# Kernel optimization log

Measured on AMD Instinct MI355X. Metric: run time of the kernel, lower is better.

The kernel has to match this reference:

```python
import jax, jax.numpy as jnp
import numpy as np

D_MODEL = 1024
N_HEAD = 16
HEAD_DIM = D_MODEL // N_HEAD
D_FF = int(D_MODEL * 4.0)
B, T = 2, 2048


def rms_norm(x, eps=1e-6):
    return x * jax.lax.rsqrt(jnp.mean(jnp.square(x), axis=-1, keepdims=True) + eps)


def rope_tables(T, head_dim):
    # half-truncated RoPE: first quarter of dims get real freqs, next quarter zeros
    angular_freq = (1.0 / 1024.0) ** jnp.linspace(0.0, 1.0, head_dim // 4, dtype=jnp.float32)
    angular_freq = jnp.concatenate([angular_freq, jnp.zeros(head_dim // 4, jnp.float32)])
    theta = jnp.arange(T, dtype=jnp.float32)[:, None] * angular_freq[None, :]  # [T, head_dim//2]
    return jnp.cos(theta), jnp.sin(theta)


def apply_rope(x, cos, sin):
    # x: [B, H, T, D]; cos/sin: [T, D//2]
    x1, x2 = jnp.split(x.astype(jnp.float32), 2, axis=-1)
    c = cos[None, None]
    s = sin[None, None]
    y1 = x1 * c + x2 * s
    y2 = -x1 * s + x2 * c
    return jnp.concatenate([y1, y2], axis=-1).astype(x.dtype)


def setup_inputs() -> dict:
    key = jax.random.key(0)
    ks = jax.random.split(key, 10)
    x = jax.random.normal(ks[0], (B, T, D_MODEL), jnp.float32)
    block_mask = jnp.tril(jnp.ones((T, T), jnp.bool_))  # causal
    sc = 1.0 / np.sqrt(D_MODEL)
    Wqkv = jax.random.normal(ks[1], (D_MODEL, 3 * D_MODEL), jnp.float32) * sc
    bqkv = jnp.zeros((3 * D_MODEL,), jnp.float32)
    Wo = jax.random.normal(ks[2], (D_MODEL, D_MODEL), jnp.float32) * sc
    bo = jnp.zeros((D_MODEL,), jnp.float32)
    W1 = jax.random.normal(ks[3], (D_MODEL, D_FF), jnp.float32) * sc
    b1 = jnp.zeros((D_FF,), jnp.float32)
    W2 = jax.random.normal(ks[4], (D_FF, D_MODEL), jnp.float32) * (1.0 / np.sqrt(D_FF))
    b2 = jnp.zeros((D_MODEL,), jnp.float32)
    return {"x": x, "block_mask": block_mask, "Wqkv": Wqkv, "bqkv": bqkv,
            "Wo": Wo, "bo": bo, "W1": W1, "b1": b1, "W2": W2, "b2": b2}


def reference(x, block_mask, Wqkv, bqkv, Wo, bo, W1, b1, W2, b2):
    Bq, Tq, D = x.shape
    cos, sin = rope_tables(Tq, HEAD_DIM)

    def attn(h):
        qkv = h @ Wqkv + bqkv  # [B, T, 3D]
        qkv = qkv.reshape(Bq, Tq, 3, N_HEAD, HEAD_DIM)
        qkv = jnp.transpose(qkv, (2, 0, 3, 1, 4))  # [3, B, H, T, d]
        q, k, v = qkv[0], qkv[1], qkv[2]
        q, k = rms_norm(q), rms_norm(k)
        q, k = apply_rope(q, cos, sin), apply_rope(k, cos, sin)
        scores = jnp.einsum('bhtd,bhsd->bhts', q, k) / np.sqrt(HEAD_DIM)
        scores = jnp.where(block_mask[None, None], scores, jnp.float32(-1e30))
        p = jax.nn.softmax(scores, axis=-1)
        o = jnp.einsum('bhts,bhsd->bhtd', p, v)
        o = jnp.transpose(o, (0, 2, 1, 3)).reshape(Bq, Tq, D)
        return o @ Wo + bo

    def mlp(h):
        return jax.nn.gelu(h @ W1 + b1) @ W2 + b2

    x = x + attn(rms_norm(x))
    x = x + mlp(rms_norm(x))
    return x
```

## Files before the change

### kernel.cpp

```cpp
#include <hip/hip_runtime.h>
#include <hip/hip_bf16.h>


typedef __attribute__((ext_vector_type(8))) short short8;
typedef __attribute__((ext_vector_type(4))) float f32x4;
typedef __attribute__((ext_vector_type(8))) unsigned short u16x8;

#define MROWS 4096
#define DMODEL 1024
#define DFF 4096
#define NH 16
#define HD 64
#define SEQ 2048

static __device__ __forceinline__ unsigned short f2bf(float f) {
    union { __hip_bfloat16 b; unsigned short u; } cv;
    cv.b = __float2bfloat16(f);
    return cv.u;
}

static __device__ __forceinline__ void gload_lds16(const void* g, void* l) {
    __builtin_amdgcn_global_load_lds(
        (const __attribute__((address_space(1))) unsigned int*)g,
        (__attribute__((address_space(3))) unsigned int*)l, 16, 0, 0);
}

__global__ void cast_transpose(const float* __restrict__ W,
                               unsigned short* __restrict__ Wt, int K, int N) {
    __shared__ float tile[32][33];
    const int tx = threadIdx.x & 31;
    const int ty = threadIdx.x >> 5;
    const int n0 = blockIdx.x * 32, k0 = blockIdx.y * 32;
#pragma unroll
    for (int i = 0; i < 4; ++i) {
        int kk = ty + i * 8;
        tile[kk][tx] = W[(long)(k0 + kk) * N + n0 + tx];
    }
    __syncthreads();
#pragma unroll
    for (int i = 0; i < 4; ++i) {
        int nn = ty + i * 8;
        Wt[(long)(n0 + nn) * K + k0 + tx] = f2bf(tile[tx][nn]);
    }
}

__global__ void rope_table(float* __restrict__ cosT, float* __restrict__ sinT) {
    const int t = blockIdx.x, j = threadIdx.x;
    float th = (j < 16) ? (float)t * exp2f(-(10.0f / 15.0f) * (float)j) : 0.0f;
    cosT[t * 32 + j] = cosf(th);
    sinT[t * 32 + j] = sinf(th);
}

__global__ void rmsnorm_cast(const float* __restrict__ xin,
                             unsigned short* __restrict__ hout) {
    const int row = blockIdx.x;
    const float4 v = ((const float4*)(xin + (long)row * DMODEL))[threadIdx.x];
    float ss = v.x * v.x + v.y * v.y + v.z * v.z + v.w * v.w;
#pragma unroll
    for (int m = 32; m >= 1; m >>= 1) ss += __shfl_xor(ss, m);
    __shared__ float part[4];
    if ((threadIdx.x & 63) == 0) part[threadIdx.x >> 6] = ss;
    __syncthreads();
    const float tot = part[0] + part[1] + part[2] + part[3];
    const float sc = rsqrtf(tot * (1.0f / (float)DMODEL) + 1e-6f);
    ushort4 o;
    o.x = f2bf(v.x * sc); o.y = f2bf(v.y * sc);
    o.z = f2bf(v.z * sc); o.w = f2bf(v.w * sc);
    ((ushort4*)hout)[(long)row * (DMODEL / 4) + threadIdx.x] = o;
}

template <int EPI>
__launch_bounds__(256)
__global__ void gemm_bt(const short* __restrict__ A, const short* __restrict__ Bt,
                        const float* __restrict__ bias, const float* __restrict__ res,
                        float* __restrict__ outF, unsigned short* __restrict__ outB,
                        int N, int K) {
    __shared__ short As[128 * 32];
    __shared__ short Bs[128 * 32];
    const int tid = threadIdx.x;
    const int lane = tid & 63, w = tid >> 6;
    const int wr = w >> 1, wc = w & 1;
    const int l16 = lane & 15, lhi = lane >> 4;
    const long rowA0 = (long)blockIdx.y * 128;
    const long rowB0 = (long)blockIdx.x * 128;

    const f32x4 fz = {0.f, 0.f, 0.f, 0.f};
    f32x4 acc[4][4];
#pragma unroll
    for (int m = 0; m < 4; ++m)
#pragma unroll
        for (int n = 0; n < 4; ++n) acc[m][n] = fz;

    const int ktiles = K >> 5;
    for (int kt = 0; kt < ktiles; ++kt) {
        const int k0 = kt << 5;
#pragma unroll
        for (int it = 0; it < 2; ++it) {
            const int cbase = it * 256 + w * 64;
            const int c = cbase + lane;
            const int r = c >> 2, col = (c & 3) << 3;
            gload_lds16(A + (rowA0 + r) * K + k0 + col,
                        (char*)As + cbase * 16 + lane * 16);
            gload_lds16(Bt + (rowB0 + r) * K + k0 + col,
                        (char*)Bs + cbase * 16 + lane * 16);
        }
        __syncthreads();
        short8 af[4], bf[4];
#pragma unroll
        for (int m = 0; m < 4; ++m)
            af[m] = *(const short8*)(As + (wr * 64 + m * 16 + l16) * 32 + lhi * 8);
#pragma unroll
        for (int n = 0; n < 4; ++n)
            bf[n] = *(const short8*)(Bs + (wc * 64 + n * 16 + l16) * 32 + lhi * 8);
#pragma unroll
        for (int m = 0; m < 4; ++m)
#pragma unroll
            for (int n = 0; n < 4; ++n)
                acc[m][n] = __builtin_amdgcn_mfma_f32_16x16x32_bf16(
                    af[m], bf[n], acc[m][n], 0, 0, 0);
        __syncthreads();
    }

#pragma unroll
    for (int m = 0; m < 4; ++m) {
        const long r0 = rowA0 + wr * 64 + m * 16 + lhi * 4;
#pragma unroll
        for (int n = 0; n < 4; ++n) {
            const long cc = rowB0 + wc * 64 + n * 16 + l16;
            const float bv = bias[cc];
#pragma unroll
            for (int j = 0; j < 4; ++j) {
                const long idx = (r0 + j) * N + cc;
                float v = acc[m][n][j] + bv;
                if (EPI == 1) v += res[idx];
                if (EPI == 2) {
                    float g = 0.5f * v *
                        (1.0f + tanhf(0.7978845608028654f * (v + 0.044715f * v * v * v)));
                    outB[idx] = f2bf(g);
                } else {
                    outF[idx] = v;
                }
            }
        }
    }
}

__global__ void qkv_post(const float* __restrict__ qkv, const float* __restrict__ cosT,
                         const float* __restrict__ sinT, unsigned short* __restrict__ Qo,
                         unsigned short* __restrict__ Ko) {
    const int lane = threadIdx.x & 63;
    const int g = blockIdx.x * 4 + (threadIdx.x >> 6);
    const int row = g >> 4, h = g & 15;
    const int b = row >> 11, t = row & 2047;
    const float* base = qkv + (long)row * 3072 + h * 64;
    float q = base[lane];
    float k = base[1024 + lane];
    float sq = q * q, sk = k * k;
#pragma unroll
    for (int m = 32; m >= 1; m >>= 1) {
        sq += __shfl_xor(sq, m);
        sk += __shfl_xor(sk, m);
    }
    q *= rsqrtf(sq * (1.0f / 64.0f) + 1e-6f);
    k *= rsqrtf(sk * (1.0f / 64.0f) + 1e-6f);
    const int j = lane & 31;
    const float c = cosT[t * 32 + j], s = sinT[t * 32 + j];
    const float q2 = __shfl_xor(q, 32), k2 = __shfl_xor(k, 32);
    const float sgn = (lane < 32) ? 1.0f : -1.0f;
    const float qr = q * c + sgn * q2 * s;
    const float kr = k * c + sgn * k2 * s;
    const long o = ((long)(b * 16 + h) * SEQ + t) * 64 + lane;
    Qo[o] = f2bf(qr * 0.125f);
    Ko[o] = f2bf(kr);
}

__global__ void transpose_v(const float* __restrict__ qkv,
                            unsigned short* __restrict__ Vt) {
    __shared__ float tile[64][65];
    const int tid = threadIdx.x;
    const int bh = blockIdx.x, tt = blockIdx.y;
    const int b = bh >> 4, h = bh & 15;
    const int tr = tid >> 2, c0 = (tid & 3) * 16;
    const float* src = qkv + ((long)(b * SEQ + tt * 64 + tr)) * 3072 + 2048 + h * 64 + c0;
#pragma unroll
    for (int i = 0; i < 4; ++i) {
        float4 v = ((const float4*)src)[i];
        tile[tr][c0 + i * 4 + 0] = v.x;
        tile[tr][c0 + i * 4 + 1] = v.y;
        tile[tr][c0 + i * 4 + 2] = v.z;
        tile[tr][c0 + i * 4 + 3] = v.w;
    }
    __syncthreads();
    const int d = tid >> 2, t0 = (tid & 3) * 16;
    unsigned short* dst = Vt + ((long)bh * 64 + d) * SEQ + tt * 64 + t0;
#pragma unroll
    for (int half = 0; half < 2; ++half) {
        u16x8 o;
#pragma unroll
        for (int e = 0; e < 8; ++e) o[e] = f2bf(tile[t0 + half * 8 + e][d]);
        *(u16x8*)(dst + half * 8) = o;
    }
}

__launch_bounds__(256)
__global__ void attn_fwd(const short* __restrict__ Qg, const short* __restrict__ Kg,
                         const short* __restrict__ Vtg, unsigned short* __restrict__ Og) {
    __shared__ short Ks[64 * 64];
    __shared__ short Vs[64 * 64];
    __shared__ char Ps[4][16 * 128];
    const int tid = threadIdx.x, lane = tid & 63, w = tid >> 6;
    const int l16 = lane & 15, lhi = lane >> 4;
    const int bh = blockIdx.x;
    const int qt = 31 - blockIdx.y;
    const int bb = bh >> 4, hh = bh & 15;
    const long base_q = (long)bh * (SEQ * 64);

    short8 aq0, aq1;
    {
        const short* Qp = Qg + base_q + (long)(qt * 64 + w * 16) * 64;
        aq0 = *(const short8*)(Qp + l16 * 64 + lhi * 8);
        aq1 = *(const short8*)(Qp + l16 * 64 + 32 + lhi * 8);
    }
    float mrow[4] = {-1e30f, -1e30f, -1e30f, -1e30f};
    float lrow[4] = {0.f, 0.f, 0.f, 0.f};
    const f32x4 fz = {0.f, 0.f, 0.f, 0.f};
    f32x4 oacc[4];
#pragma unroll
    for (int n = 0; n < 4; ++n) oacc[n] = fz;

    char* Pw = &Ps[w][0];

    for (int kt = 0; kt <= qt; ++kt) {
        const short* Kp = Kg + base_q + (long)kt * 64 * 64;
        const short* Vp = Vtg + base_q + (long)kt * 64;
#pragma unroll
        for (int it = 0; it < 2; ++it) {
            const int cbase = it * 256 + w * 64;
            const int c = cbase + lane;
            const int r = c >> 3;
            const int col = ((c & 7) ^ (r & 7)) << 3;
            gload_lds16(Kp + r * 64 + col, (char*)Ks + c * 16);
            gload_lds16(Vp + (long)r * SEQ + col, (char*)Vs + c * 16);
        }
        __syncthreads();

        f32x4 s[4];
        __builtin_amdgcn_s_setprio(1);
#pragma unroll
        for (int n = 0; n < 4; ++n) {
            const int kr = n * 16 + l16;
            short8 bk0 = *(const short8*)(Ks + kr * 64 + ((lhi ^ (kr & 7)) << 3));
            short8 bk1 = *(const short8*)(Ks + kr * 64 + (((lhi + 4) ^ (kr & 7)) << 3));
            f32x4 z = fz;
            z = __builtin_amdgcn_mfma_f32_16x16x32_bf16(aq0, bk0, z, 0, 0, 0);
            s[n] = __builtin_amdgcn_mfma_f32_16x16x32_bf16(aq1, bk1, z, 0, 0, 0);
        }
        __builtin_amdgcn_s_setprio(0);
        if (kt == qt) {
#pragma unroll
            for (int n = 0; n < 4; ++n)
#pragma unroll
                for (int j = 0; j < 4; ++j)
                    if (n * 16 + l16 > w * 16 + lhi * 4 + j) s[n][j] = -1e30f;
        }

#pragma unroll
        for (int j = 0; j < 4; ++j) {
            float pm = fmaxf(fmaxf(s[0][j], s[1][j]), fmaxf(s[2][j], s[3][j]));
            pm = fmaxf(pm, __shfl_xor(pm, 1));
            pm = fmaxf(pm, __shfl_xor(pm, 2));
            pm = fmaxf(pm, __shfl_xor(pm, 4));
            pm = fmaxf(pm, __shfl_xor(pm, 8));
            const float newm = fmaxf(mrow[j], pm);
            const float sc = __expf(mrow[j] - newm);
            float ps = 0.f;
#pragma unroll
            for (int n = 0; n < 4; ++n) {
                float p = __expf(s[n][j] - newm);
                s[n][j] = p;
                ps += p;
            }
            ps += __shfl_xor(ps, 1);
            ps += __shfl_xor(ps, 2);
            ps += __shfl_xor(ps, 4);
            ps += __shfl_xor(ps, 8);
            lrow[j] = lrow[j] * sc + ps;
            mrow[j] = newm;
#pragma unroll
            for (int n = 0; n < 4; ++n) oacc[n][j] *= sc;
        }

#pragma unroll
        for (int n = 0; n < 4; ++n)
#pragma unroll
            for (int j = 0; j < 4; ++j) {
                const int q = lhi * 4 + j, colp = n * 16 + l16;
                *(short*)(Pw + ((q * 128 + colp * 2) ^ ((q & 7) << 4))) =
                    (short)f2bf(s[n][j]);
            }
        __builtin_amdgcn_s_setprio(1);
#pragma unroll
        for (int ks = 0; ks < 2; ++ks) {
            short8 pa = *(const short8*)(Pw + ((l16 * 128 + ks * 64 + lhi * 16) ^ ((l16 & 7) << 4)));
#pragma unroll
            for (int n = 0; n < 4; ++n) {
                const int dr = n * 16 + l16;
                short8 vb = *(const short8*)(Vs + dr * 64 + ((((ks << 2) + lhi) ^ (dr & 7)) << 3));
                oacc[n] = __builtin_amdgcn_mfma_f32_16x16x32_bf16(pa, vb, oacc[n], 0, 0, 0);
            }
        }
        __builtin_amdgcn_s_setprio(0);
        __syncthreads();
    }

#pragma unroll
    for (int n = 0; n < 4; ++n)
#pragma unroll
        for (int j = 0; j < 4; ++j) {
            const int qrow = qt * 64 + w * 16 + lhi * 4 + j;
            const long orow = (long)bb * SEQ + qrow;
            const int col = hh * 64 + n * 16 + l16;
            Og[orow * DMODEL + col] = f2bf(oacc[n][j] / lrow[j]);
        }
}

extern "C" void kernel_launch(void* const* d_in, const int* in_sizes, int n_in,
                              void* d_out, int out_size, void* d_ws, size_t ws_size,
                              hipStream_t stream) {
    const float* x    = (const float*)d_in[0];
    const float* Wqkv = (const float*)d_in[2];
    const float* bqkv = (const float*)d_in[3];
    const float* Wo   = (const float*)d_in[4];
    const float* bo   = (const float*)d_in[5];
    const float* W1   = (const float*)d_in[6];
    const float* b1   = (const float*)d_in[7];
    const float* W2   = (const float*)d_in[8];
    const float* b2   = (const float*)d_in[9];
    float* out = (float*)d_out;

    char* ws = (char*)d_ws;
    auto alloc = [&](size_t b) {
        char* p = ws;
        ws += (b + 255) & ~(size_t)255;
        return p;
    };
    short* WqkvT = (short*)alloc(3072ull * 1024 * 2);
    short* WoT   = (short*)alloc(1024ull * 1024 * 2);
    short* W1T   = (short*)alloc(4096ull * 1024 * 2);
    short* W2T   = (short*)alloc(1024ull * 4096 * 2);
    float* cosT  = (float*)alloc(2048ull * 32 * 4);
    float* sinT  = (float*)alloc(2048ull * 32 * 4);
    short* hbuf  = (short*)alloc((size_t)MROWS * DMODEL * 2);
    short* Qb    = (short*)alloc(32ull * SEQ * 64 * 2);
    short* Kb    = (short*)alloc(32ull * SEQ * 64 * 2);
    short* Vtb   = (short*)alloc(32ull * 64 * SEQ * 2);
    short* Ob    = (short*)alloc((size_t)MROWS * DMODEL * 2);
    float* x1    = (float*)alloc((size_t)MROWS * DMODEL * 4);
    char*  big   = alloc((size_t)MROWS * 3072 * 4);
    float* qkv   = (float*)big;
    unsigned short* act = (unsigned short*)big;

    cast_transpose<<<dim3(96, 32), 256, 0, stream>>>(Wqkv, (unsigned short*)WqkvT, 1024, 3072);
    cast_transpose<<<dim3(32, 32), 256, 0, stream>>>(Wo, (unsigned short*)WoT, 1024, 1024);
    cast_transpose<<<dim3(128, 32), 256, 0, stream>>>(W1, (unsigned short*)W1T, 1024, 4096);
    cast_transpose<<<dim3(32, 128), 256, 0, stream>>>(W2, (unsigned short*)W2T, 4096, 1024);
    rope_table<<<2048, 32, 0, stream>>>(cosT, sinT);
    rmsnorm_cast<<<MROWS, 256, 0, stream>>>(x, (unsigned short*)hbuf);
    gemm_bt<0><<<dim3(24, 32), 256, 0, stream>>>(hbuf, WqkvT, bqkv, nullptr, qkv, nullptr, 3072, 1024);
    qkv_post<<<16384, 256, 0, stream>>>(qkv, cosT, sinT,
                                        (unsigned short*)Qb, (unsigned short*)Kb);
    transpose_v<<<dim3(32, 32), 256, 0, stream>>>(qkv, (unsigned short*)Vtb);
    attn_fwd<<<dim3(32, 32), 256, 0, stream>>>(Qb, Kb, Vtb, (unsigned short*)Ob);
    gemm_bt<1><<<dim3(8, 32), 256, 0, stream>>>(Ob, WoT, bo, x, x1, nullptr, 1024, 1024);
    rmsnorm_cast<<<MROWS, 256, 0, stream>>>(x1, (unsigned short*)hbuf);
    gemm_bt<2><<<dim3(32, 32), 256, 0, stream>>>(hbuf, W1T, b1, nullptr, nullptr, act, 4096, 1024);
    gemm_bt<1><<<dim3(8, 32), 256, 0, stream>>>((const short*)act, W2T, b2, x1, out, nullptr, 1024, 4096);
}
```

Measured before the change: 450.9 us.

## Triple-buffer GEMM LDS tiles and add XCD-aware workgroup swizzle

The GEMM now keeps three LDS buffers and issues async global-to-LDS loads two k-tiles ahead. It waits with explicit vmcnt counts and uses one barrier per iteration instead of two, so loads overlap MFMA work. Both the GEMM and attention kernels remap workgroup IDs so that consecutive logical tiles land on the same XCD, aiming for better L2 reuse. This triples LDS use in the GEMM, which may lower occupancy. The attention remap also changes the order in which causal tiles of varying length are scheduled.

```diff
diff --git a/kernel.cpp b/kernel.cpp
--- a/kernel.cpp
+++ b/kernel.cpp
@@ -23,6 +23,13 @@
     __builtin_amdgcn_global_load_lds(
         (const __attribute__((address_space(1))) unsigned int*)g,
         (__attribute__((address_space(3))) unsigned int*)l, 16, 0, 0);
+}
+
+static __device__ __forceinline__ int xcd_swizzle(int id, int nwg) {
+    const int nx = 8;
+    const int q = nwg / nx, r = nwg % nx;
+    const int xcd = id % nx, loc = id / nx;
+    return (xcd < r ? xcd * (q + 1) : r * (q + 1) + (xcd - r) * q) + loc;
 }
 
 __global__ void cast_transpose(const float* __restrict__ W,
@@ -75,14 +82,18 @@
                         const float* __restrict__ bias, const float* __restrict__ res,
                         float* __restrict__ outF, unsigned short* __restrict__ outB,
                         int N, int K) {
-    __shared__ short As[128 * 32];
-    __shared__ short Bs[128 * 32];
+    __shared__ short As[3][128 * 32];
+    __shared__ short Bs[3][128 * 32];
     const int tid = threadIdx.x;
     const int lane = tid & 63, w = tid >> 6;
     const int wr = w >> 1, wc = w & 1;
     const int l16 = lane & 15, lhi = lane >> 4;
-    const long rowA0 = (long)blockIdx.y * 128;
-    const long rowB0 = (long)blockIdx.x * 128;
+
+    const int nwg = gridDim.x * gridDim.y;
+    int id = xcd_swizzle(blockIdx.y * gridDim.x + blockIdx.x, nwg);
+    const int bx = id % gridDim.x, by = id / gridDim.x;
+    const long rowA0 = (long)by * 128;
+    const long rowB0 = (long)bx * 128;
 
     const f32x4 fz = {0.f, 0.f, 0.f, 0.f};
     f32x4 acc[4][4];
@@ -91,34 +102,54 @@
 #pragma unroll
         for (int n = 0; n < 4; ++n) acc[m][n] = fz;
 
-    const int ktiles = K >> 5;
-    for (int kt = 0; kt < ktiles; ++kt) {
+    auto stage = [&](int kt, int b) {
         const int k0 = kt << 5;
 #pragma unroll
         for (int it = 0; it < 2; ++it) {
-            const int cbase = it * 256 + w * 64;
-            const int c = cbase + lane;
+            const int c = it * 256 + w * 64 + lane;
             const int r = c >> 2, col = (c & 3) << 3;
-            gload_lds16(A + (rowA0 + r) * K + k0 + col,
-                        (char*)As + cbase * 16 + lane * 16);
-            gload_lds16(Bt + (rowB0 + r) * K + k0 + col,
-                        (char*)Bs + cbase * 16 + lane * 16);
-        }
-        __syncthreads();
+            gload_lds16(A + (rowA0 + r) * K + k0 + col, (char*)As[b] + c * 16);
+            gload_lds16(Bt + (rowB0 + r) * K + k0 + col, (char*)Bs[b] + c * 16);
+        }
+    };
+    auto compute = [&](int b) {
         short8 af[4], bf[4];
 #pragma unroll
         for (int m = 0; m < 4; ++m)
-            af[m] = *(const short8*)(As + (wr * 64 + m * 16 + l16) * 32 + lhi * 8);
+            af[m] = *(const short8*)(&As[b][0] + (wr * 64 + m * 16 + l16) * 32 + lhi * 8);
 #pragma unroll
         for (int n = 0; n < 4; ++n)
-            bf[n] = *(const short8*)(Bs + (wc * 64 + n * 16 + l16) * 32 + lhi * 8);
+            bf[n] = *(const short8*)(&Bs[b][0] + (wc * 64 + n * 16 + l16) * 32 + lhi * 8);
 #pragma unroll
         for (int m = 0; m < 4; ++m)
 #pragma unroll
             for (int n = 0; n < 4; ++n)
                 acc[m][n] = __builtin_amdgcn_mfma_f32_16x16x32_bf16(
                     af[m], bf[n], acc[m][n], 0, 0, 0);
-        __syncthreads();
+    };
+
+    const int ktiles = K >> 5;
+    stage(0, 0);
+    if (ktiles > 1) {
+        stage(1, 1);
+        asm volatile("s_waitcnt vmcnt(4)" ::: "memory");
+    } else {
+        asm volatile("s_waitcnt vmcnt(0)" ::: "memory");
+    }
+    __builtin_amdgcn_s_barrier();
+    __builtin_amdgcn_sched_barrier(0);
+
+    int b0 = 0, b1 = 1, b2 = 2;
+    for (int kt = 0; kt < ktiles; ++kt) {
+        if (kt + 2 < ktiles) stage(kt + 2, b2);
+        compute(b0);
+        if (kt + 1 < ktiles) {
+            if (kt + 2 < ktiles) asm volatile("s_waitcnt vmcnt(4)" ::: "memory");
+            else                 asm volatile("s_waitcnt vmcnt(0)" ::: "memory");
+            __builtin_amdgcn_s_barrier();
+            __builtin_amdgcn_sched_barrier(0);
+        }
+        const int t = b0; b0 = b1; b1 = b2; b2 = t;
     }
 
 #pragma unroll
@@ -210,8 +241,9 @@
     __shared__ char Ps[4][16 * 128];
     const int tid = threadIdx.x, lane = tid & 63, w = tid >> 6;
     const int l16 = lane & 15, lhi = lane >> 4;
-    const int bh = blockIdx.x;
-    const int qt = 31 - blockIdx.y;
+    int id = xcd_swizzle(blockIdx.y * gridDim.x + blockIdx.x, 1024);
+    const int bh = id >> 5;
+    const int qt = 31 - (id & 31);
     const int bb = bh >> 4, hh = bh & 15;
     const long base_q = (long)bh * (SEQ * 64);
 
@@ -235,8 +267,7 @@
         const short* Vp = Vtg + base_q + (long)kt * 64;
 #pragma unroll
         for (int it = 0; it < 2; ++it) {
-            const int cbase = it * 256 + w * 64;
-            const int c = cbase + lane;
+            const int c = it * 256 + w * 64 + lane;
             const int r = c >> 3;
             const int col = ((c & 7) ^ (r & 7)) << 3;
             gload_lds16(Kp + r * 64 + col, (char*)Ks + c * 16);
```

After: 464.1 us. 2.9% more time.
